# Kernel optimization log

Hardware: AMD Instinct MI355X
Metric: run time of the kernel (lower is better)

## Reference

```python
import jax, jax.numpy as jnp
import numpy as np

B, T, C, H = 4, 2048, 1024, 16
HS = C // H  # 64
THRESH_INIT = (5 + 1) / 12 * 0.01  # (layer_idx+1)/n_layer * final_token_threshold


def _layernorm(x, w, b, eps=1e-5):
    mu = jnp.mean(x, axis=-1, keepdims=True)
    var = jnp.var(x, axis=-1, keepdims=True)
    return (x - mu) * jax.lax.rsqrt(var + eps) * w + b


def setup_inputs() -> dict:
    key = jax.random.key(0)
    ks = jax.random.split(key, 8)
    s = 0.02
    inp = {
        'x': jax.random.normal(ks[0], (B, T, C), dtype=jnp.float32),
        'attention_mask': jnp.ones((B, T), dtype=jnp.float32),
        'protected_mask': jnp.zeros((B, T), dtype=jnp.float32),
        'ln1_w': jnp.ones((C,), jnp.float32),
        'ln1_b': jnp.zeros((C,), jnp.float32),
        'c_attn_w': jax.random.normal(ks[1], (3 * C, C), jnp.float32) * s,
        'c_attn_b': jnp.zeros((3 * C,), jnp.float32),
        'c_proj_w': jax.random.normal(ks[2], (C, C), jnp.float32) * s,
        'c_proj_b': jnp.zeros((C,), jnp.float32),
        'ln2_w': jnp.ones((C,), jnp.float32),
        'ln2_b': jnp.zeros((C,), jnp.float32),
        'fc_w': jax.random.normal(ks[3], (4 * C, C), jnp.float32) * s,
        'fc_b': jnp.zeros((4 * C,), jnp.float32),
        'fcproj_w': jax.random.normal(ks[4], (C, 4 * C), jnp.float32) * s,
        'fcproj_b': jnp.zeros((C,), jnp.float32),
        'threshold': jnp.asarray(THRESH_INIT, jnp.float32),
    }
    return inp


def reference(x, attention_mask, protected_mask, ln1_w, ln1_b, c_attn_w, c_attn_b,
              c_proj_w, c_proj_b, ln2_w, ln2_b, fc_w, fc_b, fcproj_w, fcproj_b, threshold):
    b, t, c = x.shape
    # --- attention with importance scores ---
    h = _layernorm(x, ln1_w, ln1_b)
    qkv = h @ c_attn_w.T + c_attn_b                      # (B,T,3C)
    q, k, v = jnp.split(qkv, 3, axis=-1)
    q = q.reshape(b, t, H, HS).transpose(0, 2, 1, 3)     # (B,H,T,hs)
    k = k.reshape(b, t, H, HS).transpose(0, 2, 1, 3)
    v = v.reshape(b, t, H, HS).transpose(0, 2, 1, 3)
    att = jnp.einsum('bhqd,bhkd->bhqk', q, k) / np.sqrt(HS)
    causal = jnp.tril(jnp.ones((t, t), dtype=bool))      # (T,T)
    att = jnp.where(causal[None, None], att, -jnp.inf)
    att = jnp.where(attention_mask[:, None, None, :] != 0, att, -jnp.inf)
    att = jax.nn.softmax(att, axis=-1)                   # (B,H,T,T)
    y = jnp.einsum('bhqk,bhkd->bhqd', att, v)
    y = y.transpose(0, 2, 1, 3).reshape(b, t, c)
    y = y @ c_proj_w.T + c_proj_b
    importance = att.mean(axis=1).mean(axis=1)           # (B,T): mean over heads, then queries
    # --- pruning ---
    x = x + y
    pruning_mask = (importance >= threshold).astype(x.dtype)  # hard mode
    pruning_mask = jnp.where(protected_mask > 0, jnp.ones_like(pruning_mask), pruning_mask)
    combined_mask = attention_mask * pruning_mask
    x = x * combined_mask[..., None]
    # --- MLP ---
    m = _layernorm(x, ln2_w, ln2_b)
    m = jax.nn.gelu(m @ fc_w.T + fc_b, approximate=False)
    x = x + (m @ fcproj_w.T + fcproj_b)
    pruning_loss = jnp.asarray(0.0, x.dtype)  # hard mode / lambda=0
    return (x, combined_mask, pruning_loss)
```

## Files before the change

kernel.cpp:

```cpp
#include <hip/hip_runtime.h>
#include <math.h>

#define B_ 4
#define T_ 2048
#define C_ 1024
#define H_ 16
#define NROWS (B_*T_)

typedef short s8v  __attribute__((ext_vector_type(8)));
typedef float f4v  __attribute__((ext_vector_type(4)));
typedef unsigned short u16v4 __attribute__((ext_vector_type(4)));

#define QSCALE 0.1803368801111f

static __device__ __forceinline__ unsigned short f2bf(float x) {
    unsigned u = __float_as_uint(x);
    unsigned r = u + 0x7fffu + ((u >> 16) & 1u);
    return (unsigned short)(r >> 16);
}

static __device__ __forceinline__ float fexp2(float x) {
    return __builtin_amdgcn_exp2f(x);
}

static __device__ __forceinline__ void gload_lds16(const void* g, void* l) {
    __builtin_amdgcn_global_load_lds(
        (const __attribute__((address_space(1))) void*)g,
        (__attribute__((address_space(3))) void*)l, 16, 0, 0);
}

__global__ __launch_bounds__(256) void prep_kernel(
        const float* __restrict__ x, const float* __restrict__ w,
        const float* __restrict__ b, unsigned short* __restrict__ out,
        const float* __restrict__ wsrc, unsigned short* __restrict__ wdst,
        float* __restrict__ imp, int* __restrict__ nsurv)
{
    int row = blockIdx.x;
    int tid = threadIdx.x;
    int widx = row * 96 + tid;
    if (tid < 96) {
        float4 v = ((const float4*)wsrc)[widx];
        u16v4 o = { f2bf(v.x), f2bf(v.y), f2bf(v.z), f2bf(v.w) };
        *(u16v4*)(wdst + (size_t)widx*4) = o;
    }
    if (row < 32) imp[row*256 + tid] = 0.f;
    if (row == 32 && tid < 8) nsurv[tid] = 0;

    const float4* xr = (const float4*)(x + (size_t)row * C_);
    float4 v = xr[tid];
    float s  = v.x + v.y + v.z + v.w;
    float ss = v.x*v.x + v.y*v.y + v.z*v.z + v.w*v.w;
    #pragma unroll
    for (int off = 32; off > 0; off >>= 1) {
        s  += __shfl_down(s,  off, 64);
        ss += __shfl_down(ss, off, 64);
    }
    __shared__ float rs[4], rss[4];
    __shared__ float smu, srstd;
    int wave = tid >> 6, lane = tid & 63;
    if (lane == 0) { rs[wave] = s; rss[wave] = ss; }
    __syncthreads();
    if (tid == 0) {
        float S  = rs[0]+rs[1]+rs[2]+rs[3];
        float SS = rss[0]+rss[1]+rss[2]+rss[3];
        float mu = S * (1.0f/C_);
        float var = SS * (1.0f/C_) - mu*mu;
        smu = mu; srstd = rsqrtf(var + 1e-5f);
    }
    __syncthreads();
    float mu = smu, rstd = srstd;
    float4 wv = ((const float4*)w)[tid];
    float4 bv = ((const float4*)b)[tid];
    u16v4 o;
    o.x = f2bf((v.x-mu)*rstd*wv.x + bv.x);
    o.y = f2bf((v.y-mu)*rstd*wv.y + bv.y);
    o.z = f2bf((v.z-mu)*rstd*wv.z + bv.z);
    o.w = f2bf((v.w-mu)*rstd*wv.w + bv.w);
    *(u16v4*)(out + (size_t)row * C_ + tid*4) = o;
}

__global__ __launch_bounds__(256) void ln_bf16(const float* __restrict__ x,
        const float* __restrict__ w, const float* __restrict__ b,
        unsigned short* __restrict__ out, const int* __restrict__ flag, int nrows)
{
    if (flag && flag[0] == 0) return;
    int tid = threadIdx.x;
    __shared__ float rs[4], rss[4];
    __shared__ float smu, srstd;
    int wave = tid >> 6, lane = tid & 63;
    for (int row = blockIdx.x; row < nrows; row += gridDim.x) {
        const float4* xr = (const float4*)(x + (size_t)row * C_);
        float4 v = xr[tid];
        float s  = v.x + v.y + v.z + v.w;
        float ss = v.x*v.x + v.y*v.y + v.z*v.z + v.w*v.w;
        #pragma unroll
        for (int off = 32; off > 0; off >>= 1) {
            s  += __shfl_down(s,  off, 64);
            ss += __shfl_down(ss, off, 64);
        }
        if (lane == 0) { rs[wave] = s; rss[wave] = ss; }
        __syncthreads();
        if (tid == 0) {
            float S  = rs[0]+rs[1]+rs[2]+rs[3];
            float SS = rss[0]+rss[1]+rss[2]+rss[3];
            float mu = S * (1.0f/C_);
            float var = SS * (1.0f/C_) - mu*mu;
            smu = mu; srstd = rsqrtf(var + 1e-5f);
        }
        __syncthreads();
        float mu = smu, rstd = srstd;
        float4 wv = ((const float4*)w)[tid];
        float4 bv = ((const float4*)b)[tid];
        u16v4 o;
        o.x = f2bf((v.x-mu)*rstd*wv.x + bv.x);
        o.y = f2bf((v.y-mu)*rstd*wv.y + bv.y);
        o.z = f2bf((v.z-mu)*rstd*wv.z + bv.z);
        o.w = f2bf((v.w-mu)*rstd*wv.w + bv.w);
        *(u16v4*)(out + (size_t)row * C_ + tid*4) = o;
        __syncthreads();
    }
}

__global__ __launch_bounds__(256) void cvt3_bf16(
        const float* __restrict__ cprojw, const float* __restrict__ fcw,
        const float* __restrict__ fcpw,
        unsigned short* __restrict__ wproj, unsigned short* __restrict__ wfc,
        unsigned short* __restrict__ wfcp, const int* __restrict__ flag)
{
    if (flag[0] == 0) return;
    const int total = 9*C_*C_/4;
    const int n1 = C_*C_/4;
    const int n2 = n1 + C_*C_;
    for (int i = blockIdx.x * 256 + threadIdx.x; i < total; i += gridDim.x * 256) {
        const float* src; unsigned short* dst; int j;
        if (i < n1)      { src = cprojw; dst = wproj; j = i; }
        else if (i < n2) { src = fcw;    dst = wfc;   j = i - n1; }
        else             { src = fcpw;   dst = wfcp;  j = i - n2; }
        float4 v = ((const float4*)src)[j];
        u16v4 o = { f2bf(v.x), f2bf(v.y), f2bf(v.z), f2bf(v.w) };
        *(u16v4*)(dst + (size_t)j*4) = o;
    }
}

#define STG(gbase_, ldsarr_, ah_, kt_, bb_) do { \
    gload_lds16(gbase_ + (size_t)((ah_)*128)*1024 + (kt_)*64, \
                &ldsarr_[bb_][(((ah_)*128) + (w<<3))*64]); \
    gload_lds16(gbase_ + (size_t)((ah_)*128 + 64)*1024 + (kt_)*64, \
                &ldsarr_[bb_][(((ah_)*128 + 64) + (w<<3))*64]); \
} while (0)

#define PHASE(ah_, bh_, ...) do { \
    s8v af[4][2], bf[2][2]; \
    _Pragma("unroll") \
    for (int i2 = 0; i2 < 4; i2++) { \
        int arow = ((ah_)*128 + wr*64 + i2*16 + l16)*64; \
        af[i2][0] = *(const s8v*)&As[bb][arow + (((quad)     ^ (l16&7))<<3)]; \
        af[i2][1] = *(const s8v*)&As[bb][arow + (((4 + quad) ^ (l16&7))<<3)]; \
    } \
    _Pragma("unroll") \
    for (int j2 = 0; j2 < 2; j2++) { \
        int brow = ((bh_)*128 + wc*32 + j2*16 + l16)*64; \
        bf[j2][0] = *(const s8v*)&Bs[bb][brow + (((quad)     ^ (l16&7))<<3)]; \
        bf[j2][1] = *(const s8v*)&Bs[bb][brow + (((4 + quad) ^ (l16&7))<<3)]; \
    } \
    __VA_ARGS__; \
    asm volatile("s_barrier" ::: "memory"); \
    asm volatile("s_waitcnt lgkmcnt(0)" ::: "memory"); \
    __builtin_amdgcn_sched_barrier(0); \
    __builtin_amdgcn_s_setprio(1); \
    _Pragma("unroll") \
    for (int i2 = 0; i2 < 4; i2++) \
        _Pragma("unroll") \
        for (int j2 = 0; j2 < 2; j2++) { \
            acc[(ah_)*4+i2][(bh_)*2+j2] = __builtin_amdgcn_mfma_f32_16x16x32_bf16( \
                af[i2][0], bf[j2][0], acc[(ah_)*4+i2][(bh_)*2+j2], 0, 0, 0); \
            acc[(ah_)*4+i2][(bh_)*2+j2] = __builtin_amdgcn_mfma_f32_16x16x32_bf16( \
                af[i2][1], bf[j2][1], acc[(ah_)*4+i2][(bh_)*2+j2], 0, 0, 0); \
        } \
    __builtin_amdgcn_s_setprio(0); \
    __builtin_amdgcn_sched_barrier(0); \
    asm volatile("s_barrier" ::: "memory"); \
} while (0)

__global__ __launch_bounds__(512, 2) void gemm_qk_8ph(
    const unsigned short* __restrict__ A,
    const unsigned short* __restrict__ Bw,
    const float* __restrict__ bias,
    unsigned short* __restrict__ qh, unsigned short* __restrict__ kh)
{
    __shared__ unsigned short As[2][256*64];
    __shared__ unsigned short Bs[2][256*64];

    const int tid  = threadIdx.x;
    const int w    = tid >> 6, lane = tid & 63;
    const int quad = lane >> 4, l16 = lane & 15;
    const int wr   = w >> 2, wc = w & 3;
    const int rl   = tid >> 3;
    const int kc   = (tid & 7) ^ (rl & 7);

    const int bid = blockIdx.x;
    const int vb  = (bid & 7) * 32 + (bid >> 3);
    const int m0  = (vb >> 3) << 8;
    const int n0  = (vb & 7) << 8;

    const unsigned short* gA0 = A  + (size_t)(m0 + rl) * 1024 + kc * 8;
    const unsigned short* gB0 = Bw + (size_t)(n0 + rl) * 1024 + kc * 8;

    STG(gA0, As, 0, 0, 0);
    STG(gB0, Bs, 1, 0, 0);
    STG(gA0, As, 1, 0, 0);
    STG(gB0, Bs, 0, 0, 0);
    STG(gA0, As, 0, 1, 1);
    STG(gB0, Bs, 1, 1, 1);

    f4v acc[8][4];
    #pragma unroll
    for (int i = 0; i < 8; i++)
        #pragma unroll
        for (int j = 0; j < 4; j++) {
            acc[i][j][0] = 0.f; acc[i][j][1] = 0.f;
            acc[i][j][2] = 0.f; acc[i][j][3] = 0.f;
        }

    #pragma unroll 2
    for (int t = 0; t < 16; ++t) {
        const int bb = t & 1, nb = bb ^ 1;
        if (t < 15) asm volatile("s_waitcnt vmcnt(4)" ::: "memory");
        else        asm volatile("s_waitcnt vmcnt(0)" ::: "memory");
        asm volatile("s_barrier" ::: "memory");
        __builtin_amdgcn_sched_barrier(0);
        PHASE(0, 0, if (t < 15) STG(gA0, As, 1, t+1, nb));
        PHASE(0, 1, if (t < 15) STG(gB0, Bs, 0, t+1, nb));
        PHASE(1, 1, if (t < 14) STG(gA0, As, 0, t+2, bb));
        PHASE(1, 0, if (t < 14) STG(gB0, Bs, 1, t+2, bb));
    }

    #pragma unroll
    for (int j = 0; j < 4; j++) {
        int ncol = n0 + ((j >> 1) << 7) + (wc << 5) + ((j & 1) << 4) + l16;
        float bv = bias[ncol];
        int sec = ncol >> 10;
        int hh = (ncol & 1023) >> 6, dd = ncol & 63;
        unsigned short* basep = (sec == 0) ? qh : kh;
        bool qsec = (sec == 0);
        #pragma unroll
        for (int i = 0; i < 8; i++) {
            int mbase = m0 + ((i >> 2) << 7) + (wr << 6) + ((i & 3) << 4) + (quad << 2);
            #pragma unroll
            for (int reg = 0; reg < 4; reg++) {
                int m = mbase + reg;
                float v = acc[i][j][reg] + bv;
                if (qsec) v *= QSCALE;
                int b_ = m >> 11, tt = m & 2047;
                basep[(((size_t)(b_*H_ + hh))*T_ + tt)*64 + dd] = f2bf(v);
            }
        }
    }
}

template<int EPI>
__global__ __launch_bounds__(256) void gemm_bf16(
    const unsigned short* __restrict__ A,
    const unsigned short* __restrict__ Bw,
    const float* __restrict__ bias,
    const float* __restrict__ res,
    float* __restrict__ Cout, unsigned short* __restrict__ Cbf,
    int K, int lda, int ldb, int ldc, int ncoff,
    const float* __restrict__ cmv,
    unsigned short* __restrict__ qh, unsigned short* __restrict__ kh,
    unsigned short* __restrict__ vh, const int* __restrict__ flag,
    int nbx, int nby)
{
    if (flag && flag[0] == 0) return;
    __shared__ unsigned short As[128*64];
    __shared__ unsigned short Bs[128*64];
    int tid = threadIdx.x;
    int w = tid >> 6, lane = tid & 63, quad = lane >> 4, l16 = lane & 15;
    int wr = w >> 1, wc = w & 1;

    int nvb = nbx * nby;
    int vb0 = blockIdx.y * gridDim.x + blockIdx.x;
    int vstride = gridDim.x * gridDim.y;

    for (int vb = vb0; vb < nvb; vb += vstride) {
        int n0 = (vb % nbx) * 128;
        int m0 = (vb / nbx) * 128;

        size_t offA[4], offB[4];
        #pragma unroll
        for (int j = 0; j < 4; j++) {
            int ci = j*256 + tid;
            int mr = ci >> 3, kcs = ci & 7;
            int kc = kcs ^ (mr & 7);
            offA[j] = (size_t)(m0 + mr) * lda + kc*8;
            offB[j] = (size_t)(n0 + mr) * ldb + kc*8;
        }

        f4v acc[4][4];
        #pragma unroll
        for (int i = 0; i < 4; i++)
            #pragma unroll
            for (int j = 0; j < 4; j++) { acc[i][j][0]=0.f; acc[i][j][1]=0.f; acc[i][j][2]=0.f; acc[i][j][3]=0.f; }

        for (int k0 = 0; k0 < K; k0 += 64) {
            __syncthreads();
            #pragma unroll
            for (int j = 0; j < 4; j++) {
                gload_lds16(A  + offA[j] + k0, &As[(j*256 + (w<<6))*8]);
                gload_lds16(Bw + offB[j] + k0, &Bs[(j*256 + (w<<6))*8]);
            }
            __syncthreads();
            #pragma unroll
            for (int c = 0; c < 2; c++) {
                s8v af[4], bf[4];
                int sw = ((c<<2) + quad) ^ (l16 & 7);
                #pragma unroll
                for (int i = 0; i < 4; i++) {
                    int mr = wr*64 + i*16 + l16;
                    af[i] = *(const s8v*)&As[mr*64 + sw*8];
                    int nr = wc*64 + i*16 + l16;
                    bf[i] = *(const s8v*)&Bs[nr*64 + sw*8];
                }
                #pragma unroll
                for (int i = 0; i < 4; i++)
                    #pragma unroll
                    for (int j = 0; j < 4; j++)
                        acc[i][j] = __builtin_amdgcn_mfma_f32_16x16x32_bf16(af[i], bf[j], acc[i][j], 0, 0, 0);
            }
        }

        #pragma unroll
        for (int j = 0; j < 4; j++) {
            int ncol = n0 + wc*64 + j*16 + l16;
            float bv = bias ? bias[ncol] : 0.f;
            int hh = 0, dd = 0;
            bool qsec = false;
            unsigned short* basep = nullptr;
            if (EPI == 3) {
                int ncolg = ncol + ncoff;
                int sec = ncolg >> 10;
                int hn = ncolg & 1023;
                hh = hn >> 6; dd = hn & 63;
                basep = (sec == 0) ? qh : (sec == 1) ? kh : vh;
                qsec = (sec == 0);
            }
            #pragma unroll
            for (int i = 0; i < 4; i++) {
                #pragma unroll
                for (int reg = 0; reg < 4; reg++) {
                    int m = m0 + wr*64 + i*16 + quad*4 + reg;
                    float v = acc[i][j][reg] + bv;
                    if (EPI == 1) {
                        v = 0.5f * v * (1.0f + erff(v * 0.70710678118654752f));
                        Cbf[(size_t)m*ldc + ncol] = f2bf(v);
                    } else if (EPI == 2) {
                        Cout[(size_t)m*ldc + ncol] = v + res[(size_t)m*ldc + ncol];
                    } else if (EPI == 3) {
                        if (qsec) v *= QSCALE;
                        int bb = m >> 11, t = m & 2047;
                        basep[(((size_t)(bb*H_ + hh))*T_ + t)*64 + dd] = f2bf(v);
                    } else if (EPI == 4) {
                        Cout[(size_t)m*ldc + ncol] = (res[(size_t)m*ldc + ncol] + v) * cmv[m];
                    }
                }
            }
        }
    }
}

#define RS_LOADK(K_, it_) do { \
    int k0_ = (it_) * 64; \
    _Pragma("unroll") \
    for (int c_ = 0; c_ < 2; c_++) \
        _Pragma("unroll") \
        for (int nt_ = 0; nt_ < 4; nt_++) \
            K_[c_][nt_] = *(const s8v*)(kp + (size_t)(k0_ + nt_*16 + l16)*64 + c_*32 + quad*8); \
} while (0)

#define RS_COMP(K_, it_) do { \
    int k0_ = (it_) * 64; \
    float mk[4]; \
    _Pragma("unroll") \
    for (int nt_ = 0; nt_ < 4; nt_++) mk[nt_] = msk01[k0_ + nt_*16 + l16]; \
    bool allm = __all(mk[0] != 0.f && mk[1] != 0.f && mk[2] != 0.f && mk[3] != 0.f); \
    _Pragma("unroll") \
    for (int qf = 0; qf < 4; qf++) { \
        f4v acc[4]; \
        _Pragma("unroll") \
        for (int nt_ = 0; nt_ < 4; nt_++) { acc[nt_][0]=0.f; acc[nt_][1]=0.f; acc[nt_][2]=0.f; acc[nt_][3]=0.f; } \
        _Pragma("unroll") \
        for (int c_ = 0; c_ < 2; c_++) \
            _Pragma("unroll") \
            for (int nt_ = 0; nt_ < 4; nt_++) \
                acc[nt_] = __builtin_amdgcn_mfma_f32_16x16x32_bf16(aQ[qf][c_], K_[c_][nt_], acc[nt_], 0, 0, 0); \
        if ((it_) < qt && allm) { \
            _Pragma("unroll") \
            for (int nt_ = 0; nt_ < 4; nt_++) \
                _Pragma("unroll") \
                for (int reg = 0; reg < 4; reg++) \
                    lrow[qf][reg] += fexp2(acc[nt_][reg]); \
        } else if ((it_) < qt) { \
            _Pragma("unroll") \
            for (int nt_ = 0; nt_ < 4; nt_++) \
                _Pragma("unroll") \
                for (int reg = 0; reg < 4; reg++) \
                    lrow[qf][reg] += fexp2(acc[nt_][reg]) * mk[nt_]; \
        } else { \
            _Pragma("unroll") \
            for (int nt_ = 0; nt_ < 4; nt_++) { \
                int kg = k0_ + nt_*16 + l16; \
                _Pragma("unroll") \
                for (int reg = 0; reg < 4; reg++) { \
                    float me = (kg <= q0 + qf*16 + quad*4 + reg) ? mk[nt_] : 0.f; \
                    lrow[qf][reg] += fexp2(acc[nt_][reg]) * me; \
                } \
            } \
        } \
    } \
} while (0)

__global__ __launch_bounds__(256) void attn_rowsum(
    const unsigned short* __restrict__ qh, const unsigned short* __restrict__ kh,
    const float* __restrict__ amask, float* __restrict__ linvbuf)
{
    __shared__ float msk01[2048];
    __shared__ float lred[4][64];

    int tid = threadIdx.x;
    int w = tid >> 6, lane = tid & 63, quad = lane >> 4, l16 = lane & 15;
    int qt = 31 - (blockIdx.x >> 6);
    int bh = blockIdx.x & 63;
    int b  = bh >> 4;
    int q0 = qt * 64;
    int ntiles = qt + 1;

    const unsigned short* qp = qh + (size_t)bh*T_*64;
    const unsigned short* kp = kh + (size_t)bh*T_*64;
    const float* amp = amask + b*T_;

    for (int i = tid; i < ntiles*64; i += 256)
        msk01[i] = (amp[i] != 0.f) ? 1.f : 0.f;

    s8v aQ[4][2];
    #pragma unroll
    for (int qf = 0; qf < 4; qf++) {
        int row = q0 + qf*16 + l16;
        aQ[qf][0] = *(const s8v*)(qp + (size_t)row*64 + quad*8);
        aQ[qf][1] = *(const s8v*)(qp + (size_t)row*64 + 32 + quad*8);
    }

    float lrow[4][4];
    #pragma unroll
    for (int qf = 0; qf < 4; qf++)
        #pragma unroll
        for (int reg = 0; reg < 4; reg++) lrow[qf][reg] = 0.f;

    s8v K0[2][4], K1[2][4];
    int it = w;
    if (it < ntiles) RS_LOADK(K0, it);
    __syncthreads();
    if (it < ntiles) {
        while (true) {
            int itn = it + 4;
            if (itn < ntiles) {
                RS_LOADK(K1, itn);
                RS_COMP(K0, it);
                int it2 = itn + 4;
                if (it2 < ntiles) {
                    RS_LOADK(K0, it2);
                    RS_COMP(K1, itn);
                    it = it2;
                    continue;
                } else {
                    RS_COMP(K1, itn);
                    break;
                }
            } else {
                RS_COMP(K0, it);
                break;
            }
        }
    }

    #pragma unroll
    for (int qf = 0; qf < 4; qf++)
        #pragma unroll
        for (int reg = 0; reg < 4; reg++) {
            float v = lrow[qf][reg];
            v += __shfl_xor(v, 1); v += __shfl_xor(v, 2);
            v += __shfl_xor(v, 4); v += __shfl_xor(v, 8);
            lrow[qf][reg] = v;
        }
    if (l16 == 0) {
        #pragma unroll
        for (int qf = 0; qf < 4; qf++)
            #pragma unroll
            for (int reg = 0; reg < 4; reg++)
                lred[w][qf*16 + quad*4 + reg] = lrow[qf][reg];
    }
    __syncthreads();
    if (tid < 64) {
        float t = lred[0][tid] + lred[1][tid] + lred[2][tid] + lred[3][tid];
        linvbuf[(size_t)bh*T_ + q0 + tid] = (t > 0.f) ? 1.0f / t : 0.f;
    }
}

#define CS_LOADQT(AQ_, LV_, qt_) do { \
    _Pragma("unroll") \
    for (int qf_ = 0; qf_ < 4; qf_++) { \
        int row_ = (qt_)*64 + qf_*16 + l16; \
        AQ_[qf_][0] = *(const s8v*)(qp + (size_t)row_*64 + quad*8); \
        AQ_[qf_][1] = *(const s8v*)(qp + (size_t)row_*64 + 32 + quad*8); \
        LV_[qf_] = *(const float4*)(lp + (qt_)*64 + qf_*16 + quad*4); \
    } \
} while (0)

#define CS_COMPQT(AQ_, LV_, qt_) do { \
    if ((qt_) > kc) { \
        _Pragma("unroll") \
        for (int qf_ = 0; qf_ < 4; qf_++) { \
            f4v acc[4]; \
            _Pragma("unroll") \
            for (int nt_ = 0; nt_ < 4; nt_++) { acc[nt_][0]=0.f; acc[nt_][1]=0.f; acc[nt_][2]=0.f; acc[nt_][3]=0.f; } \
            _Pragma("unroll") \
            for (int nt_ = 0; nt_ < 4; nt_++) { \
                acc[nt_] = __builtin_amdgcn_mfma_f32_16x16x32_bf16(AQ_[qf_][0], bk[0][nt_], acc[nt_], 0, 0, 0); \
                acc[nt_] = __builtin_amdgcn_mfma_f32_16x16x32_bf16(AQ_[qf_][1], bk[1][nt_], acc[nt_], 0, 0, 0); \
            } \
            float lv[4] = { LV_[qf_].x, LV_[qf_].y, LV_[qf_].z, LV_[qf_].w }; \
            _Pragma("unroll") \
            for (int nt_ = 0; nt_ < 4; nt_++) \
                _Pragma("unroll") \
                for (int reg = 0; reg < 4; reg++) \
                    cs[nt_] += fexp2(acc[nt_][reg]) * lv[reg]; \
        } \
    } else { \
        _Pragma("unroll") \
        for (int qf_ = 0; qf_ < 4; qf_++) { \
            f4v acc[4]; \
            _Pragma("unroll") \
            for (int nt_ = 0; nt_ < 4; nt_++) { acc[nt_][0]=0.f; acc[nt_][1]=0.f; acc[nt_][2]=0.f; acc[nt_][3]=0.f; } \
            _Pragma("unroll") \
            for (int nt_ = 0; nt_ < 4; nt_++) { \
                acc[nt_] = __builtin_amdgcn_mfma_f32_16x16x32_bf16(AQ_[qf_][0], bk[0][nt_], acc[nt_], 0, 0, 0); \
                acc[nt_] = __builtin_amdgcn_mfma_f32_16x16x32_bf16(AQ_[qf_][1], bk[1][nt_], acc[nt_], 0, 0, 0); \
            } \
            float lv[4] = { LV_[qf_].x, LV_[qf_].y, LV_[qf_].z, LV_[qf_].w }; \
            _Pragma("unroll") \
            for (int nt_ = 0; nt_ < 4; nt_++) { \
                int kg = k0 + nt_*16 + l16; \
                _Pragma("unroll") \
                for (int reg = 0; reg < 4; reg++) { \
                    float me = (kg <= (qt_)*64 + qf_*16 + quad*4 + reg) ? 1.f : 0.f; \
                    cs[nt_] += fexp2(acc[nt_][reg]) * lv[reg] * me; \
                } \
            } \
        } \
    } \
} while (0)

__global__ __launch_bounds__(256) void attn_colsum(
    const unsigned short* __restrict__ qh, const unsigned short* __restrict__ kh,
    const float* __restrict__ amask, const float* __restrict__ linvbuf,
    float* __restrict__ imp)
{
    __shared__ float cred[4][64];

    int tid = threadIdx.x;
    int w = tid >> 6, lane = tid & 63, quad = lane >> 4, l16 = lane & 15;
    int kc = blockIdx.x >> 6;
    int bh = blockIdx.x & 63;
    int b  = bh >> 4;
    int k0 = kc * 64;

    const unsigned short* qp = qh + (size_t)bh*T_*64;
    const unsigned short* kp = kh + (size_t)bh*T_*64;
    const float* lp = linvbuf + (size_t)bh*T_;

    s8v bk[2][4];
    float mk[4];
    #pragma unroll
    for (int nt = 0; nt < 4; nt++) {
        int key = k0 + nt*16 + l16;
        bk[0][nt] = *(const s8v*)(kp + (size_t)key*64 + quad*8);
        bk[1][nt] = *(const s8v*)(kp + (size_t)key*64 + 32 + quad*8);
        mk[nt] = amask[b*T_ + key];
    }

    float cs[4] = {0.f, 0.f, 0.f, 0.f};

    int qt = kc + w;
    if (qt < 32) {
        s8v AQa[4][2], AQb[4][2];
        float4 LVa[4], LVb[4];
        CS_LOADQT(AQa, LVa, qt);
        while (true) {
            int qtn = qt + 4;
            if (qtn < 32) {
                CS_LOADQT(AQb, LVb, qtn);
                CS_COMPQT(AQa, LVa, qt);
                int qt2 = qtn + 4;
                if (qt2 < 32) {
                    CS_LOADQT(AQa, LVa, qt2);
                    CS_COMPQT(AQb, LVb, qtn);
                    qt = qt2;
                    continue;
                } else {
                    CS_COMPQT(AQb, LVb, qtn);
                    break;
                }
            } else {
                CS_COMPQT(AQa, LVa, qt);
                break;
            }
        }
    }

    #pragma unroll
    for (int nt = 0; nt < 4; nt++) {
        float v = cs[nt] * mk[nt];
        v += __shfl_xor(v, 16);
        v += __shfl_xor(v, 32);
        if (quad == 0) cred[w][nt*16 + l16] = v;
    }
    __syncthreads();
    if (tid < 64)
        atomicAdd(&imp[b*T_ + k0 + tid],
                  cred[0][tid] + cred[1][tid] + cred[2][tid] + cred[3][tid]);
}

__global__ __launch_bounds__(256) void mask_finalize(
    const float* __restrict__ imp, const float* __restrict__ amask,
    const float* __restrict__ prot, const float* __restrict__ thr,
    float* __restrict__ mask_out, float* __restrict__ loss_out,
    int* __restrict__ nsurv)
{
    int i = blockIdx.x * 256 + threadIdx.x;
    float impv = imp[i] * (1.0f / (float)(H_ * T_));
    float pm = (impv >= thr[0]) ? 1.f : 0.f;
    if (prot[i] > 0.f) pm = 1.f;
    float cm = amask[i] * pm;
    mask_out[i] = cm;
    if (i == 0) loss_out[0] = 0.f;
    unsigned long long bal = __ballot(cm != 0.f);
    int cnt = __popcll(bal);
    __shared__ int bs;
    if (threadIdx.x == 0) bs = 0;
    __syncthreads();
    if ((threadIdx.x & 63) == 0 && cnt) atomicAdd(&bs, cnt);
    __syncthreads();
    if (threadIdx.x == 0 && bs) atomicAdd(nsurv, bs);
}

__global__ __launch_bounds__(256) void attn_full(
    const unsigned short* __restrict__ qh, const unsigned short* __restrict__ kh,
    const unsigned short* __restrict__ vh, const float* __restrict__ amask,
    unsigned short* __restrict__ y, const int* __restrict__ flag)
{
    if (flag[0] == 0) return;
    __shared__ unsigned short Ks[64][72];
    __shared__ unsigned short Vt[64][72];
    __shared__ unsigned short Ps[4][16][72];
    __shared__ float mks[64];

    int tid = threadIdx.x;
    int w = tid >> 6, lane = tid & 63, quad = lane >> 4, l16 = lane & 15;
    int nqt = T_ / 64;

    for (int vb = blockIdx.x; vb < B_*H_*nqt; vb += gridDim.x) {
        int qt = vb % nqt;
        int bh = vb / nqt;
        int b = bh >> 4, h = bh & 15;
        int q0 = qt * 64;

        const unsigned short* qp = qh + (size_t)bh * T_ * 64;
        const unsigned short* kp = kh + (size_t)bh * T_ * 64;
        const unsigned short* vp = vh + (size_t)bh * T_ * 64;

        int qrow = q0 + 16*w + l16;
        s8v aQ0 = *(const s8v*)(qp + (size_t)qrow*64 + quad*8);
        s8v aQ1 = *(const s8v*)(qp + (size_t)qrow*64 + 32 + quad*8);

        int qwmax = q0 + 16*w + 15;
        int ntiles = qt + 1;
        int qg = q0 + 16*w + quad*4;

        float lrow[4] = {0.f, 0.f, 0.f, 0.f};
        for (int it = 0; it < ntiles; ++it) {
            int k0 = it * 64;
            __syncthreads();
            for (int cid = tid; cid < 512; cid += 256) {
                int row = cid >> 3, ch = cid & 7;
                *(s8v*)&Ks[row][ch*8] = *(const s8v*)(kp + (size_t)(k0+row)*64 + ch*8);
            }
            if (tid < 64) mks[tid] = amask[b*T_ + k0 + tid];
            __syncthreads();
            if (k0 > qwmax) continue;
            f4v accS[4];
            #pragma unroll
            for (int nt = 0; nt < 4; nt++) { accS[nt][0]=0.f; accS[nt][1]=0.f; accS[nt][2]=0.f; accS[nt][3]=0.f; }
            #pragma unroll
            for (int nt = 0; nt < 4; nt++) {
                s8v b0 = *(const s8v*)&Ks[nt*16 + l16][quad*8];
                s8v b1 = *(const s8v*)&Ks[nt*16 + l16][32 + quad*8];
                accS[nt] = __builtin_amdgcn_mfma_f32_16x16x32_bf16(aQ0, b0, accS[nt], 0, 0, 0);
                accS[nt] = __builtin_amdgcn_mfma_f32_16x16x32_bf16(aQ1, b1, accS[nt], 0, 0, 0);
            }
            #pragma unroll
            for (int nt = 0; nt < 4; nt++) {
                int kg = k0 + nt*16 + l16;
                float mkv = mks[nt*16 + l16];
                #pragma unroll
                for (int reg = 0; reg < 4; reg++) {
                    bool val = (kg <= qg + reg) && (mkv != 0.f);
                    float e = fexp2(accS[nt][reg]);
                    lrow[reg] += val ? e : 0.f;
                }
            }
        }
        float linv[4];
        #pragma unroll
        for (int reg = 0; reg < 4; reg++) {
            float v = lrow[reg];
            v += __shfl_xor(v, 1); v += __shfl_xor(v, 2);
            v += __shfl_xor(v, 4); v += __shfl_xor(v, 8);
            linv[reg] = (v > 0.f) ? 1.0f / v : 0.f;
        }

        f4v accO[4];
        #pragma unroll
        for (int nt = 0; nt < 4; nt++) { accO[nt][0]=0.f; accO[nt][1]=0.f; accO[nt][2]=0.f; accO[nt][3]=0.f; }

        for (int it = 0; it < ntiles; ++it) {
            int k0 = it * 64;
            __syncthreads();
            for (int cid = tid; cid < 512; cid += 256) {
                int row = cid >> 3, ch = cid & 7;
                s8v kv = *(const s8v*)(kp + (size_t)(k0+row)*64 + ch*8);
                *(s8v*)&Ks[row][ch*8] = kv;
                s8v vv = *(const s8v*)(vp + (size_t)(k0+row)*64 + ch*8);
                #pragma unroll
                for (int j = 0; j < 8; j++) Vt[ch*8 + j][row] = (unsigned short)vv[j];
            }
            if (tid < 64) mks[tid] = amask[b*T_ + k0 + tid];
            __syncthreads();
            if (k0 > qwmax) continue;
            f4v accS[4];
            #pragma unroll
            for (int nt = 0; nt < 4; nt++) { accS[nt][0]=0.f; accS[nt][1]=0.f; accS[nt][2]=0.f; accS[nt][3]=0.f; }
            #pragma unroll
            for (int nt = 0; nt < 4; nt++) {
                s8v b0 = *(const s8v*)&Ks[nt*16 + l16][quad*8];
                s8v b1 = *(const s8v*)&Ks[nt*16 + l16][32 + quad*8];
                accS[nt] = __builtin_amdgcn_mfma_f32_16x16x32_bf16(aQ0, b0, accS[nt], 0, 0, 0);
                accS[nt] = __builtin_amdgcn_mfma_f32_16x16x32_bf16(aQ1, b1, accS[nt], 0, 0, 0);
            }
            #pragma unroll
            for (int nt = 0; nt < 4; nt++) {
                int kg = k0 + nt*16 + l16;
                float mkv = mks[nt*16 + l16];
                #pragma unroll
                for (int reg = 0; reg < 4; reg++) {
                    bool val = (kg <= qg + reg) && (mkv != 0.f);
                    float p = val ? fexp2(accS[nt][reg]) * linv[reg] : 0.f;
                    Ps[w][quad*4 + reg][nt*16 + l16] = f2bf(p);
                }
            }
            s8v aP0 = *(const s8v*)&Ps[w][l16][quad*8];
            s8v aP1 = *(const s8v*)&Ps[w][l16][32 + quad*8];
            #pragma unroll
            for (int nt = 0; nt < 4; nt++) {
                s8v bv0 = *(const s8v*)&Vt[nt*16 + l16][quad*8];
                s8v bv1 = *(const s8v*)&Vt[nt*16 + l16][32 + quad*8];
                accO[nt] = __builtin_amdgcn_mfma_f32_16x16x32_bf16(aP0, bv0, accO[nt], 0, 0, 0);
                accO[nt] = __builtin_amdgcn_mfma_f32_16x16x32_bf16(aP1, bv1, accO[nt], 0, 0, 0);
            }
        }
        #pragma unroll
        for (int nt = 0; nt < 4; nt++) {
            #pragma unroll
            for (int reg = 0; reg < 4; reg++) {
                int q = q0 + 16*w + quad*4 + reg;
                y[((size_t)(b*T_ + q))*C_ + h*64 + nt*16 + l16] = f2bf(accO[nt][reg]);
            }
        }
        __syncthreads();
    }
}

__global__ __launch_bounds__(256) void ap_fc(const int* __restrict__ nsurv,
        const float* __restrict__ ln2b, const float* __restrict__ fcw,
        const float* __restrict__ fcb, float* __restrict__ abuf)
{
    if (nsurv[0] != 0) return;
    int j = blockIdx.x * 4 + (threadIdx.x >> 6);
    int lane = threadIdx.x & 63;
    const float4* wr = (const float4*)(fcw + (size_t)j * C_);
    const float4* bb = (const float4*)ln2b;
    float s = 0.f;
    #pragma unroll
    for (int k = 0; k < 4; k++) {
        float4 a = bb[lane + 64*k];
        float4 wv = wr[lane + 64*k];
        s += a.x*wv.x + a.y*wv.y + a.z*wv.z + a.w*wv.w;
    }
    #pragma unroll
    for (int off = 32; off > 0; off >>= 1) s += __shfl_down(s, off, 64);
    if (lane == 0) {
        float v = fcb[j] + s;
        abuf[j] = 0.5f * v * (1.0f + erff(v * 0.70710678118654752f));
    }
}

__global__ __launch_bounds__(256) void ap_fcp(const int* __restrict__ nsurv,
        const float* __restrict__ abuf, const float* __restrict__ fcpw,
        const float* __restrict__ fcpb, float* __restrict__ rowbuf)
{
    if (nsurv[0] != 0) return;
    int c = blockIdx.x * 4 + (threadIdx.x >> 6);
    int lane = threadIdx.x & 63;
    const float4* wr = (const float4*)(fcpw + (size_t)c * (4*C_));
    const float4* ab = (const float4*)abuf;
    float s = 0.f;
    #pragma unroll
    for (int k = 0; k < 16; k++) {
        float4 a = ab[lane + 64*k];
        float4 wv = wr[lane + 64*k];
        s += a.x*wv.x + a.y*wv.y + a.z*wv.z + a.w*wv.w;
    }
    #pragma unroll
    for (int off = 32; off > 0; off >>= 1) s += __shfl_down(s, off, 64);
    if (lane == 0) rowbuf[c] = fcpb[c] + s;
}

__global__ __launch_bounds__(256) void ap_bcast(const int* __restrict__ nsurv,
        const float* __restrict__ rowbuf, float* __restrict__ out_x)
{
    if (nsurv[0] != 0) return;
    float4 v = ((const float4*)rowbuf)[threadIdx.x];
    for (int r = blockIdx.x; r < NROWS; r += gridDim.x)
        ((float4*)(out_x + (size_t)r * C_))[threadIdx.x] = v;
}

extern "C" void kernel_launch(void* const* d_in, const int* in_sizes, int n_in,
                              void* d_out, int out_size, void* d_ws, size_t ws_size,
                              hipStream_t stream) {
    const float* x       = (const float*)d_in[0];
    const float* amask   = (const float*)d_in[1];
    const float* prot    = (const float*)d_in[2];
    const float* ln1w    = (const float*)d_in[3];
    const float* ln1b    = (const float*)d_in[4];
    const float* cattn_w = (const float*)d_in[5];
    const float* cattn_b = (const float*)d_in[6];
    const float* cproj_w = (const float*)d_in[7];
    const float* cproj_b = (const float*)d_in[8];
    const float* ln2w    = (const float*)d_in[9];
    const float* ln2b    = (const float*)d_in[10];
    const float* fcw     = (const float*)d_in[11];
    const float* fcb     = (const float*)d_in[12];
    const float* fcpw    = (const float*)d_in[13];
    const float* fcpb    = (const float*)d_in[14];
    const float* thr     = (const float*)d_in[15];

    unsigned short* wqkv  = (unsigned short*)d_ws;
    unsigned short* wproj = wqkv  + (size_t)3*C_*C_;
    unsigned short* wfc   = wproj + (size_t)C_*C_;
    unsigned short* wfcp  = wfc   + (size_t)4*C_*C_;
    unsigned short* hbuf  = wfcp  + (size_t)4*C_*C_;
    unsigned short* qh    = hbuf  + (size_t)NROWS*C_;
    unsigned short* kh    = qh    + (size_t)NROWS*C_;
    unsigned short* vh    = kh    + (size_t)NROWS*C_;
    unsigned short* cbuf  = qh;
    float* imp    = (float*)(vh + (size_t)NROWS*C_);
    int*   nsurv  = (int*)(imp + NROWS);
    float* abuf   = (float*)(nsurv + 8);
    float* rowbuf = abuf + 4*C_;
    float* linvbuf = rowbuf + C_;

    float* out_x    = (float*)d_out;
    float* out_mask = out_x + (size_t)NROWS*C_;
    float* out_loss = out_mask + NROWS;

    hipLaunchKernelGGL(prep_kernel, dim3(NROWS), dim3(256), 0, stream,
                       x, ln1w, ln1b, hbuf, cattn_w, wqkv, imp, nsurv);
    hipLaunchKernelGGL(gemm_qk_8ph, dim3(256), dim3(512), 0, stream,
                       hbuf, wqkv, cattn_b, qh, kh);
    hipLaunchKernelGGL(attn_rowsum, dim3(64*32), dim3(256), 0, stream,
                       qh, kh, amask, linvbuf);
    hipLaunchKernelGGL(attn_colsum, dim3(64*32), dim3(256), 0, stream,
                       qh, kh, amask, linvbuf, imp);
    hipLaunchKernelGGL(mask_finalize, dim3(NROWS/256), dim3(256), 0, stream,
                       imp, amask, prot, thr, out_mask, out_loss, nsurv);

    hipLaunchKernelGGL(cvt3_bf16, dim3(512), dim3(256), 0, stream,
                       cproj_w, fcw, fcpw, wproj, wfc, wfcp, nsurv);
    hipLaunchKernelGGL((gemm_bf16<3>), dim3(512), dim3(256), 0, stream,
                       hbuf, wqkv + (size_t)2048*C_, cattn_b + 2048, nullptr, nullptr, nullptr,
                       C_, C_, C_, 0, 2048, nullptr, qh, kh, vh, nsurv, 8, 64);
    hipLaunchKernelGGL(attn_full, dim3(512), dim3(256), 0, stream,
                       qh, kh, vh, amask, hbuf, nsurv);
    hipLaunchKernelGGL((gemm_bf16<4>), dim3(512), dim3(256), 0, stream,
                       hbuf, wproj, cproj_b, x, out_x, nullptr,
                       C_, C_, C_, C_, 0, out_mask, nullptr, nullptr, nullptr, nsurv, 8, 64);
    hipLaunchKernelGGL(ln_bf16, dim3(512), dim3(256), 0, stream,
                       out_x, ln2w, ln2b, hbuf, nsurv, NROWS);
    for (int j = 0; j < 2; j++) {
        hipLaunchKernelGGL((gemm_bf16<1>), dim3(512), dim3(256), 0, stream,
                           hbuf, wfc + (size_t)j*2048*C_, fcb + j*2048, nullptr, nullptr, cbuf,
                           C_, C_, C_, 2048, 0, nullptr, nullptr, nullptr, nullptr, nsurv, 16, 64);
        hipLaunchKernelGGL((gemm_bf16<2>), dim3(512), dim3(256), 0, stream,
                           cbuf, wfcp + (size_t)j*2048, (j == 0) ? fcpb : nullptr, out_x, out_x, nullptr,
                           2048, 2048, 4*C_, C_, 0, nullptr, nullptr, nullptr, nullptr, nsurv, 8, 64);
    }

    hipLaunchKernelGGL(ap_fc,    dim3(4*C_/4), dim3(256), 0, stream, nsurv, ln2b, fcw, fcb, abuf);
    hipLaunchKernelGGL(ap_fcp,   dim3(C_/4),   dim3(256), 0, stream, nsurv, abuf, fcpw, fcpb, rowbuf);
    hipLaunchKernelGGL(ap_bcast, dim3(512),    dim3(256), 0, stream, nsurv, rowbuf, out_x);
}
```

Measured before the change: 306.1 us.

## Double per-block query/key tile size in attention row and column sum kernels

The rowsum kernel now gives each block 128 query rows (8 fragments) instead of 64, and the colsum kernel gives each block 128 keys (8 key fragments) instead of 64. Both grids are halved, and each K or Q tile loaded is reused across twice as many MFMAs, which cuts redundant global loads. The first MFMA now takes a zero constant instead of an explicitly zeroed accumulator. The trade-off is higher register pressure, which may lower occupancy, and fewer blocks to balance the causal triangle across CUs.

Measured after the change: 310.3 us. No clear change (+1.4%).

```diff
diff --git a/kernel.cpp b/kernel.cpp
--- a/kernel.cpp
+++ b/kernel.cpp
@@ -384,22 +384,20 @@
     for (int nt_ = 0; nt_ < 4; nt_++) mk[nt_] = msk01[k0_ + nt_*16 + l16]; \
     bool allm = __all(mk[0] != 0.f && mk[1] != 0.f && mk[2] != 0.f && mk[3] != 0.f); \
     _Pragma("unroll") \
-    for (int qf = 0; qf < 4; qf++) { \
+    for (int qf = 0; qf < 8; qf++) { \
         f4v acc[4]; \
         _Pragma("unroll") \
-        for (int nt_ = 0; nt_ < 4; nt_++) { acc[nt_][0]=0.f; acc[nt_][1]=0.f; acc[nt_][2]=0.f; acc[nt_][3]=0.f; } \
-        _Pragma("unroll") \
-        for (int c_ = 0; c_ < 2; c_++) \
-            _Pragma("unroll") \
-            for (int nt_ = 0; nt_ < 4; nt_++) \
-                acc[nt_] = __builtin_amdgcn_mfma_f32_16x16x32_bf16(aQ[qf][c_], K_[c_][nt_], acc[nt_], 0, 0, 0); \
-        if ((it_) < qt && allm) { \
+        for (int nt_ = 0; nt_ < 4; nt_++) { \
+            acc[nt_] = __builtin_amdgcn_mfma_f32_16x16x32_bf16(aQ[qf][0], K_[0][nt_], ZACC, 0, 0, 0); \
+            acc[nt_] = __builtin_amdgcn_mfma_f32_16x16x32_bf16(aQ[qf][1], K_[1][nt_], acc[nt_], 0, 0, 0); \
+        } \
+        if ((it_) < diag0 && allm) { \
             _Pragma("unroll") \
             for (int nt_ = 0; nt_ < 4; nt_++) \
                 _Pragma("unroll") \
                 for (int reg = 0; reg < 4; reg++) \
                     lrow[qf][reg] += fexp2(acc[nt_][reg]); \
-        } else if ((it_) < qt) { \
+        } else if ((it_) < diag0) { \
             _Pragma("unroll") \
             for (int nt_ = 0; nt_ < 4; nt_++) \
                 _Pragma("unroll") \
@@ -424,15 +422,16 @@
     const float* __restrict__ amask, float* __restrict__ linvbuf)
 {
     __shared__ float msk01[2048];
-    __shared__ float lred[4][64];
+    __shared__ float lred[4][128];
 
     int tid = threadIdx.x;
     int w = tid >> 6, lane = tid & 63, quad = lane >> 4, l16 = lane & 15;
-    int qt = 31 - (blockIdx.x >> 6);
+    int s  = 15 - (blockIdx.x >> 6);
     int bh = blockIdx.x & 63;
     int b  = bh >> 4;
-    int q0 = qt * 64;
-    int ntiles = qt + 1;
+    int q0 = s * 128;
+    int diag0 = 2*s;
+    int ntiles = 2*s + 2;
 
     const unsigned short* qp = qh + (size_t)bh*T_*64;
     const unsigned short* kp = kh + (size_t)bh*T_*64;
@@ -441,19 +440,21 @@
     for (int i = tid; i < ntiles*64; i += 256)
         msk01[i] = (amp[i] != 0.f) ? 1.f : 0.f;
 
-    s8v aQ[4][2];
-    #pragma unroll
-    for (int qf = 0; qf < 4; qf++) {
+    s8v aQ[8][2];
+    #pragma unroll
+    for (int qf = 0; qf < 8; qf++) {
         int row = q0 + qf*16 + l16;
         aQ[qf][0] = *(const s8v*)(qp + (size_t)row*64 + quad*8);
         aQ[qf][1] = *(const s8v*)(qp + (size_t)row*64 + 32 + quad*8);
     }
 
-    float lrow[4][4];
-    #pragma unroll
-    for (int qf = 0; qf < 4; qf++)
+    float lrow[8][4];
+    #pragma unroll
+    for (int qf = 0; qf < 8; qf++)
         #pragma unroll
         for (int reg = 0; reg < 4; reg++) lrow[qf][reg] = 0.f;
+
+    const f4v ZACC = {0.f, 0.f, 0.f, 0.f};
 
     s8v K0[2][4], K1[2][4];
     int it = w;
@@ -483,7 +484,7 @@
     }
 
     #pragma unroll
-    for (int qf = 0; qf < 4; qf++)
+    for (int qf = 0; qf < 8; qf++)
         #pragma unroll
         for (int reg = 0; reg < 4; reg++) {
             float v = lrow[qf][reg];
@@ -493,43 +494,41 @@
         }
     if (l16 == 0) {
         #pragma unroll
-        for (int qf = 0; qf < 4; qf++)
+        for (int qf = 0; qf < 8; qf++)
             #pragma unroll
             for (int reg = 0; reg < 4; reg++)
                 lred[w][qf*16 + quad*4 + reg] = lrow[qf][reg];
     }
     __syncthreads();
-    if (tid < 64) {
+    if (tid < 128) {
         float t = lred[0][tid] + lred[1][tid] + lred[2][tid] + lred[3][tid];
         linvbuf[(size_t)bh*T_ + q0 + tid] = (t > 0.f) ? 1.0f / t : 0.f;
     }
 }
 
-#define CS_LOADQT(AQ_, LV_, qt_) do { \
+#define CS_LOADQT(AQ_, LV_, rt_) do { \
     _Pragma("unroll") \
     for (int qf_ = 0; qf_ < 4; qf_++) { \
-        int row_ = (qt_)*64 + qf_*16 + l16; \
+        int row_ = (rt_)*64 + qf_*16 + l16; \
         AQ_[qf_][0] = *(const s8v*)(qp + (size_t)row_*64 + quad*8); \
         AQ_[qf_][1] = *(const s8v*)(qp + (size_t)row_*64 + 32 + quad*8); \
-        LV_[qf_] = *(const float4*)(lp + (qt_)*64 + qf_*16 + quad*4); \
+        LV_[qf_] = *(const float4*)(lp + (rt_)*64 + qf_*16 + quad*4); \
     } \
 } while (0)
 
-#define CS_COMPQT(AQ_, LV_, qt_) do { \
-    if ((qt_) > kc) { \
+#define CS_COMPQT(AQ_, LV_, rt_) do { \
+    if ((rt_) > diagmax) { \
         _Pragma("unroll") \
         for (int qf_ = 0; qf_ < 4; qf_++) { \
-            f4v acc[4]; \
+            f4v acc[8]; \
             _Pragma("unroll") \
-            for (int nt_ = 0; nt_ < 4; nt_++) { acc[nt_][0]=0.f; acc[nt_][1]=0.f; acc[nt_][2]=0.f; acc[nt_][3]=0.f; } \
-            _Pragma("unroll") \
-            for (int nt_ = 0; nt_ < 4; nt_++) { \
-                acc[nt_] = __builtin_amdgcn_mfma_f32_16x16x32_bf16(AQ_[qf_][0], bk[0][nt_], acc[nt_], 0, 0, 0); \
+            for (int nt_ = 0; nt_ < 8; nt_++) { \
+                acc[nt_] = __builtin_amdgcn_mfma_f32_16x16x32_bf16(AQ_[qf_][0], bk[0][nt_], ZACC, 0, 0, 0); \
                 acc[nt_] = __builtin_amdgcn_mfma_f32_16x16x32_bf16(AQ_[qf_][1], bk[1][nt_], acc[nt_], 0, 0, 0); \
             } \
             float lv[4] = { LV_[qf_].x, LV_[qf_].y, LV_[qf_].z, LV_[qf_].w }; \
             _Pragma("unroll") \
-            for (int nt_ = 0; nt_ < 4; nt_++) \
+            for (int nt_ = 0; nt_ < 8; nt_++) \
                 _Pragma("unroll") \
                 for (int reg = 0; reg < 4; reg++) \
                     cs[nt_] += fexp2(acc[nt_][reg]) * lv[reg]; \
@@ -537,21 +536,19 @@
     } else { \
         _Pragma("unroll") \
         for (int qf_ = 0; qf_ < 4; qf_++) { \
-            f4v acc[4]; \
+            f4v acc[8]; \
             _Pragma("unroll") \
-            for (int nt_ = 0; nt_ < 4; nt_++) { acc[nt_][0]=0.f; acc[nt_][1]=0.f; acc[nt_][2]=0.f; acc[nt_][3]=0.f; } \
-            _Pragma("unroll") \
-            for (int nt_ = 0; nt_ < 4; nt_++) { \
-                acc[nt_] = __builtin_amdgcn_mfma_f32_16x16x32_bf16(AQ_[qf_][0], bk[0][nt_], acc[nt_], 0, 0, 0); \
+            for (int nt_ = 0; nt_ < 8; nt_++) { \
+                acc[nt_] = __builtin_amdgcn_mfma_f32_16x16x32_bf16(AQ_[qf_][0], bk[0][nt_], ZACC, 0, 0, 0); \
                 acc[nt_] = __builtin_amdgcn_mfma_f32_16x16x32_bf16(AQ_[qf_][1], bk[1][nt_], acc[nt_], 0, 0, 0); \
             } \
             float lv[4] = { LV_[qf_].x, LV_[qf_].y, LV_[qf_].z, LV_[qf_].w }; \
             _Pragma("unroll") \
-            for (int nt_ = 0; nt_ < 4; nt_++) { \
+            for (int nt_ = 0; nt_ < 8; nt_++) { \
                 int kg = k0 + nt_*16 + l16; \
                 _Pragma("unroll") \
                 for (int reg = 0; reg < 4; reg++) { \
-                    float me = (kg <= (qt_)*64 + qf_*16 + quad*4 + reg) ? 1.f : 0.f; \
+                    float me = (kg <= (rt_)*64 + qf_*16 + quad*4 + reg) ? 1.f : 0.f; \
                     cs[nt_] += fexp2(acc[nt_][reg]) * lv[reg] * me; \
                 } \
             } \
@@ -564,67 +561,69 @@
     const float* __restrict__ amask, const float* __restrict__ linvbuf,
     float* __restrict__ imp)
 {
-    __shared__ float cred[4][64];
+    __shared__ float cred[4][128];
 
     int tid = threadIdx.x;
     int w = tid >> 6, lane = tid & 63, quad = lane >> 4, l16 = lane & 15;
     int kc = blockIdx.x >> 6;
     int bh = blockIdx.x & 63;
     int b  = bh >> 4;
-    int k0 = kc * 64;
+    int k0 = kc * 128;
+    int diagmax = 2*kc + 1;
 
     const unsigned short* qp = qh + (size_t)bh*T_*64;
     const unsigned short* kp = kh + (size_t)bh*T_*64;
     const float* lp = linvbuf + (size_t)bh*T_;
 
-    s8v bk[2][4];
-    float mk[4];
-    #pragma unroll
-    for (int nt = 0; nt < 4; nt++) {
+    s8v bk[2][8];
+    float mk[8];
+    #pragma unroll
+    for (int nt = 0; nt < 8; nt++) {
         int key = k0 + nt*16 + l16;
         bk[0][nt] = *(const s8v*)(kp + (size_t)key*64 + quad*8);
         bk[1][nt] = *(const s8v*)(kp + (size_t)key*64 + 32 + quad*8);
         mk[nt] = amask[b*T_ + key];
     }
 
-    float cs[4] = {0.f, 0.f, 0.f, 0.f};
-
-    int qt = kc + w;
-    if (qt < 32) {
+    float cs[8] = {0.f, 0.f, 0.f, 0.f, 0.f, 0.f, 0.f, 0.f};
+    const f4v ZACC = {0.f, 0.f, 0.f, 0.f};
+
+    int rt = 2*kc + w;
+    if (rt < 32) {
         s8v AQa[4][2], AQb[4][2];
         float4 LVa[4], LVb[4];
-        CS_LOADQT(AQa, LVa, qt);
+        CS_LOADQT(AQa, LVa, rt);
         while (true) {
-            int qtn = qt + 4;
-            if (qtn < 32) {
-                CS_LOADQT(AQb, LVb, qtn);
-                CS_COMPQT(AQa, LVa, qt);
-                int qt2 = qtn + 4;
-                if (qt2 < 32) {
-                    CS_LOADQT(AQa, LVa, qt2);
-                    CS_COMPQT(AQb, LVb, qtn);
-                    qt = qt2;
+            int rtn = rt + 4;
+            if (rtn < 32) {
+                CS_LOADQT(AQb, LVb, rtn);
+                CS_COMPQT(AQa, LVa, rt);
+                int rt2 = rtn + 4;
+                if (rt2 < 32) {
+                    CS_LOADQT(AQa, LVa, rt2);
+                    CS_COMPQT(AQb, LVb, rtn);
+                    rt = rt2;
                     continue;
                 } else {
-                    CS_COMPQT(AQb, LVb, qtn);
+                    CS_COMPQT(AQb, LVb, rtn);
                     break;
                 }
             } else {
-                CS_COMPQT(AQa, LVa, qt);
+                CS_COMPQT(AQa, LVa, rt);
                 break;
             }
         }
     }
 
     #pragma unroll
-    for (int nt = 0; nt < 4; nt++) {
+    for (int nt = 0; nt < 8; nt++) {
         float v = cs[nt] * mk[nt];
         v += __shfl_xor(v, 16);
         v += __shfl_xor(v, 32);
         if (quad == 0) cred[w][nt*16 + l16] = v;
     }
     __syncthreads();
-    if (tid < 64)
+    if (tid < 128)
         atomicAdd(&imp[b*T_ + k0 + tid],
                   cred[0][tid] + cred[1][tid] + cred[2][tid] + cred[3][tid]);
 }
@@ -885,9 +884,9 @@
                        x, ln1w, ln1b, hbuf, cattn_w, wqkv, imp, nsurv);
     hipLaunchKernelGGL(gemm_qk_8ph, dim3(256), dim3(512), 0, stream,
                        hbuf, wqkv, cattn_b, qh, kh);
-    hipLaunchKernelGGL(attn_rowsum, dim3(64*32), dim3(256), 0, stream,
+    hipLaunchKernelGGL(attn_rowsum, dim3(64*16), dim3(256), 0, stream,
                        qh, kh, amask, linvbuf);
-    hipLaunchKernelGGL(attn_colsum, dim3(64*32), dim3(256), 0, stream,
+    hipLaunchKernelGGL(attn_colsum, dim3(64*16), dim3(256), 0, stream,
                        qh, kh, amask, linvbuf, imp);
     hipLaunchKernelGGL(mask_finalize, dim3(NROWS/256), dim3(256), 0, stream,
                        imp, amask, prot, thr, out_mask, out_loss, nsurv);
```
